# Kernel optimization log

Measured on AMD Instinct MI355X. Metric: run time of the kernel, lower is better.

## Reference

```python
import jax, jax.numpy as jnp
import numpy as np

B, S, D = 4, 2048, 1024
EPS = 1e-6


def setup_inputs() -> dict:
    key = jax.random.key(0)
    ks = jax.random.split(key, 9)
    s = 1.0 / np.sqrt(D)
    return {
        "context": jax.random.normal(ks[0], (B, S, D), jnp.float32),
        "eos_mask": jax.random.randint(ks[1], (B, S, S), 0, 2, dtype=jnp.int32),
        "prior": jax.random.uniform(ks[2], (B, S, S), jnp.float32),
        "Wq": jax.random.uniform(ks[3], (D, D), jnp.float32, -s, s),
        "bq": jax.random.uniform(ks[4], (D,), jnp.float32, -s, s),
        "Wk": jax.random.uniform(ks[5], (D, D), jnp.float32, -s, s),
        "bk": jax.random.uniform(ks[6], (D,), jnp.float32, -s, s),
        "gamma": jnp.ones((D,), jnp.float32),
        "beta": jnp.zeros((D,), jnp.float32),
    }


def reference(context, eos_mask, prior, Wq, bq, Wk, bk, gamma, beta):
    d = context.shape[-1]
    seq = context.shape[1]

    # LayerNorm with torch's unbiased std (Bessel correction)
    mean = jnp.mean(context, axis=-1, keepdims=True)
    var = jnp.sum((context - mean) ** 2, axis=-1, keepdims=True) / (d - 1)
    x = gamma * (context - mean) / (jnp.sqrt(var) + EPS) + beta

    q = x @ Wq + bq  # linear_query
    k = x @ Wk + bk  # linear_key

    scores = jnp.einsum("bid,bjd->bij", q, k) / d  # note: /d, not /sqrt(d)

    idx = jnp.arange(seq)
    band = jnp.abs(idx[:, None] - idx[None, :]) == 1      # a + c (tridiagonal off-diagonals)
    sup = (idx[None, :] - idx[:, None]) == 1              # a (superdiagonal)
    strict_upper = idx[:, None] < idx[None, :]            # triu(ones) - eye
    eye = idx[:, None] == idx[None, :]

    mask = (eos_mask != 0) & band[None]                   # eos_mask & (a + c)
    scores = jnp.where(mask, scores, -1e9)
    na = jax.nn.softmax(scores, axis=-1)
    na = jnp.sqrt(na * jnp.swapaxes(na, -1, -2) + 1e-9)
    na = prior + (1.0 - prior) * na                       # hier_add_index branch

    # t = log(na+eps).masked_fill(a==0,0) @ triu  ==  cumsum along last axis
    t = jnp.where(sup[None], jnp.log(na + 1e-9), 0.0)
    t = jnp.cumsum(t, axis=-1)
    # g = triu @ t  ==  reversed cumsum along axis -2
    g = jnp.cumsum(t[..., ::-1, :], axis=-2)[..., ::-1, :]
    g = jnp.where(strict_upper[None], jnp.exp(g), 0.0)

    g_attn = g + jnp.swapaxes(g, -1, -2) + jnp.where(eye[None], na, 1e-9)
    return (g_attn, na)
```

## Files before the change

### kernel.cpp

```cpp
#include <hip/hip_runtime.h>
#include <hip/hip_bf16.h>
#include <cmath>

#define BB 4
#define SS 2048
#define DD 1024
#define BS (BB*SS)
constexpr float EPS = 1e-6f;

typedef __attribute__((ext_vector_type(8))) short short8;
typedef __attribute__((ext_vector_type(4))) float floatx4;

__device__ inline float bf2f(unsigned short u) {
    unsigned v = ((unsigned)u) << 16;
    float f; __builtin_memcpy(&f, &v, 4);
    return f;
}

__global__ __launch_bounds__(256)
void prep_kernel(const float* __restrict__ Wq, const float* __restrict__ Wk,
                 const float* __restrict__ bq, const float* __restrict__ bk,
                 __hip_bfloat16* __restrict__ Wb, float* __restrict__ u,
                 float* __restrict__ v, float* __restrict__ cs,
                 float* __restrict__ sacc) {
    int blk = blockIdx.x;
    if (blk < 2048) {
        int idx = blk * 256 + threadIdx.x;
        const int half = DD * DD / 4;
        const float* src = (idx < half) ? Wk : Wq;
        int off = (idx < half) ? idx : idx - half;
        float4 val = ((const float4*)src)[off];
        union { ushort4 uu; __hip_bfloat16 h[4]; } pk;
        pk.h[0] = __float2bfloat16(val.x);
        pk.h[1] = __float2bfloat16(val.y);
        pk.h[2] = __float2bfloat16(val.z);
        pk.h[3] = __float2bfloat16(val.w);
        ((ushort4*)Wb)[idx] = pk.uu;
    } else if (blk < 2561) {
        int gid = (blk - 2048) * 4 + (threadIdx.x >> 6);
        int lane = threadIdx.x & 63;
        if (gid > 2048) return;
        const float* row; const float* vec; float* outp;
        if (gid < 1024)      { row = Wq + (size_t)gid * DD;          vec = bk; outp = u + gid; }
        else if (gid < 2048) { row = Wk + (size_t)(gid - 1024) * DD; vec = bq; outp = v + (gid - 1024); }
        else                 { row = bq;                             vec = bk; outp = cs; }
        float s = 0.f;
        #pragma unroll
        for (int k = 0; k < 4; ++k) {
            float4 a = ((const float4*)row)[lane * 4 + k];
            float4 b = ((const float4*)vec)[lane * 4 + k];
            s += a.x * b.x + a.y * b.y + a.z * b.z + a.w * b.w;
        }
        #pragma unroll
        for (int off = 32; off; off >>= 1) s += __shfl_down(s, off);
        if (lane == 0) *outp = s;
    } else {
        int idx = (blk - 2561) * 1024 + threadIdx.x * 4;
        *(float4*)(sacc + idx) = make_float4(0.f, 0.f, 0.f, 0.f);
    }
}

__global__ __launch_bounds__(256)
void ln_kernel(const float* __restrict__ ctx, const float* __restrict__ gamma,
               const float* __restrict__ beta, const float* __restrict__ u,
               const float* __restrict__ v, const float* __restrict__ cs,
               __hip_bfloat16* __restrict__ xo, float* __restrict__ alpha,
               float* __restrict__ betav) {
    int row = blockIdx.x;
    int t = threadIdx.x;
    const float* r = ctx + (size_t)row * DD;
    float4 val = ((const float4*)r)[t];
    float s1 = val.x + val.y + val.z + val.w;
    float s2 = val.x*val.x + val.y*val.y + val.z*val.z + val.w*val.w;
    #pragma unroll
    for (int off = 32; off; off >>= 1) {
        s1 += __shfl_down(s1, off);
        s2 += __shfl_down(s2, off);
    }
    __shared__ float ls1[4], ls2[4];
    int wid = t >> 6, lane = t & 63;
    if (lane == 0) { ls1[wid] = s1; ls2[wid] = s2; }
    __syncthreads();
    if (t == 0) {
        float a = ls1[0] + ls1[1] + ls1[2] + ls1[3];
        float b = ls2[0] + ls2[1] + ls2[2] + ls2[3];
        float mean = a / DD;
        float var = (b - a * a / DD) / (DD - 1);
        ls1[0] = mean;
        ls2[0] = 1.0f / (sqrtf(var) + EPS);
    }
    __syncthreads();
    float mean = ls1[0], rstd = ls2[0];
    float4 g = ((const float4*)gamma)[t];
    float4 be = ((const float4*)beta)[t];
    float nx0 = g.x * (val.x - mean) * rstd + be.x;
    float nx1 = g.y * (val.y - mean) * rstd + be.y;
    float nx2 = g.z * (val.z - mean) * rstd + be.z;
    float nx3 = g.w * (val.w - mean) * rstd + be.w;
    union { ushort4 uu; __hip_bfloat16 h[4]; } pk;
    pk.h[0] = __float2bfloat16(nx0);
    pk.h[1] = __float2bfloat16(nx1);
    pk.h[2] = __float2bfloat16(nx2);
    pk.h[3] = __float2bfloat16(nx3);
    ((ushort4*)(xo + (size_t)row * DD))[t] = pk.uu;
    float4 u4 = ((const float4*)u)[t];
    float4 v4 = ((const float4*)v)[t];
    float du = nx0 * u4.x + nx1 * u4.y + nx2 * u4.z + nx3 * u4.w;
    float dv = nx0 * v4.x + nx1 * v4.y + nx2 * v4.z + nx3 * v4.w;
    #pragma unroll
    for (int off = 32; off; off >>= 1) {
        du += __shfl_down(du, off);
        dv += __shfl_down(dv, off);
    }
    __syncthreads();
    if (lane == 0) { ls1[wid] = du; ls2[wid] = dv; }
    __syncthreads();
    if (t == 0) {
        alpha[row] = ls1[0] + ls1[1] + ls1[2] + ls1[3] + *cs;
        betav[row] = ls2[0] + ls2[1] + ls2[2] + ls2[3];
    }
}

__global__ __launch_bounds__(256)
void gemm64_mfma(const __hip_bfloat16* __restrict__ A,
                 const __hip_bfloat16* __restrict__ B,
                 __hip_bfloat16* __restrict__ C, int ldc) {
    __shared__ short As[64 * 64];
    __shared__ short Bs[64 * 64];
    int tid = threadIdx.x;
    int wave = tid >> 6;
    int lane = tid & 63;
    int q = lane >> 4, m16 = lane & 15;
    int srow = lane >> 3;
    int skoff = ((lane & 7) ^ srow) * 8;

    const __hip_bfloat16* gA = A + ((size_t)blockIdx.x * 64 + wave * 16 + srow) * DD + skoff;
    const __hip_bfloat16* gB = B + ((size_t)blockIdx.y * 64 + wave * 16 + srow) * DD + skoff;
    short* lA0 = As + (wave * 16) * 64;
    short* lA1 = As + (wave * 16 + 8) * 64;
    short* lB0 = Bs + (wave * 16) * 64;
    short* lB1 = Bs + (wave * 16 + 8) * 64;

    int swr = (m16 & 7) * 8;

    floatx4 acc[4] = {};
    for (int k0 = 0; k0 < DD; k0 += 64) {
        __builtin_amdgcn_global_load_lds(
            (const __attribute__((address_space(1))) void*)(gA + k0),
            (__attribute__((address_space(3))) void*)(lA0), 16, 0, 0);
        __builtin_amdgcn_global_load_lds(
            (const __attribute__((address_space(1))) void*)(gA + k0 + 8 * DD),
            (__attribute__((address_space(3))) void*)(lA1), 16, 0, 0);
        __builtin_amdgcn_global_load_lds(
            (const __attribute__((address_space(1))) void*)(gB + k0),
            (__attribute__((address_space(3))) void*)(lB0), 16, 0, 0);
        __builtin_amdgcn_global_load_lds(
            (const __attribute__((address_space(1))) void*)(gB + k0 + 8 * DD),
            (__attribute__((address_space(3))) void*)(lB1), 16, 0, 0);
        __syncthreads();
        #pragma unroll
        for (int h = 0; h < 2; ++h) {
            short8 af = *(const short8*)(As + (wave * 16 + m16) * 64 + ((h * 32 + q * 8) ^ swr));
            #pragma unroll
            for (int c = 0; c < 4; ++c) {
                short8 bf_ = *(const short8*)(Bs + (c * 16 + m16) * 64 + ((h * 32 + q * 8) ^ swr));
                acc[c] = __builtin_amdgcn_mfma_f32_16x16x32_bf16(af, bf_, acc[c], 0, 0, 0);
            }
        }
        __syncthreads();
    }
    #pragma unroll
    for (int c = 0; c < 4; ++c) {
        int gcol = blockIdx.y * 64 + c * 16 + m16;
        #pragma unroll
        for (int e = 0; e < 4; ++e) {
            int grow = blockIdx.x * 64 + wave * 16 + q * 4 + e;
            C[(size_t)grow * ldc + gcol] = __float2bfloat16(acc[c][e]);
        }
    }
}

#define TM 128
#define TN 128
#define BK 64
__global__ __launch_bounds__(256)
void gemm2_fused(const __hip_bfloat16* __restrict__ A,
                 const __hip_bfloat16* __restrict__ B,
                 float* __restrict__ sacc) {
    __shared__ short smem[32768];
    int tid = threadIdx.x;
    int wave = tid >> 6;
    int lane = tid & 63;
    int wm = wave >> 1, wn = wave & 1;
    int q = lane >> 4, m16 = lane & 15;

    int srow = lane >> 3;
    int skoff = ((lane & 7) ^ srow) * 8;
    const __hip_bfloat16* gA = A + ((size_t)blockIdx.x * TM + wave * 32 + srow) * DD + skoff;
    const __hip_bfloat16* gB = B + ((size_t)blockIdx.y * TN + wave * 32 + srow) * DD + skoff;

    int swr = (m16 & 7) * 8;

    floatx4 acc[4][4] = {};

    #define STAGE(p, k0) do {                                                        \
        short* As_ = smem + (p) * 16384;                                             \
        short* Bs_ = As_ + 8192;                                                     \
        _Pragma("unroll")                                                            \
        for (int i_ = 0; i_ < 4; ++i_) {                                             \
            __builtin_amdgcn_global_load_lds(                                        \
                (const __attribute__((address_space(1))) void*)(gA + (k0) + i_ * 8 * DD), \
                (__attribute__((address_space(3))) void*)(As_ + (wave * 32 + i_ * 8) * BK), 16, 0, 0); \
            __builtin_amdgcn_global_load_lds(                                        \
                (const __attribute__((address_space(1))) void*)(gB + (k0) + i_ * 8 * DD), \
                (__attribute__((address_space(3))) void*)(Bs_ + (wave * 32 + i_ * 8) * BK), 16, 0, 0); \
        }                                                                            \
    } while (0)

    #define COMPUTE(p) do {                                                          \
        const short* As_ = smem + (p) * 16384;                                       \
        const short* Bs_ = As_ + 8192;                                               \
        _Pragma("unroll")                                                            \
        for (int kk = 0; kk < 2; ++kk) {                                             \
            short8 af[4], bfr[4];                                                    \
            _Pragma("unroll")                                                        \
            for (int r = 0; r < 4; ++r)                                              \
                af[r] = *(const short8*)(As_ + (wm * 64 + r * 16 + m16) * BK + ((kk * 32 + q * 8) ^ swr)); \
            _Pragma("unroll")                                                        \
            for (int c = 0; c < 4; ++c)                                              \
                bfr[c] = *(const short8*)(Bs_ + (wn * 64 + c * 16 + m16) * BK + ((kk * 32 + q * 8) ^ swr)); \
            _Pragma("unroll")                                                        \
            for (int r = 0; r < 4; ++r)                                              \
                _Pragma("unroll")                                                    \
                for (int c = 0; c < 4; ++c)                                          \
                    acc[r][c] = __builtin_amdgcn_mfma_f32_16x16x32_bf16(af[r], bfr[c], acc[r][c], 0, 0, 0); \
        }                                                                            \
    } while (0)

    STAGE(0, 0);
    __syncthreads();
    for (int t = 0; t < DD / BK; t += 2) {
        if (t + 1 < DD / BK) STAGE(1, (t + 1) * BK);
        COMPUTE(0);
        __syncthreads();
        if (t + 2 < DD / BK) STAGE(0, (t + 2) * BK);
        COMPUTE(1);
        __syncthreads();
    }
    #undef STAGE
    #undef COMPUTE

    short* EP = smem + wave * 4608;
    #pragma unroll
    for (int r = 0; r < 4; ++r)
        #pragma unroll
        for (int c = 0; c < 4; ++c)
            #pragma unroll
            for (int e = 0; e < 4; ++e) {
                __hip_bfloat16 hv = __float2bfloat16(acc[r][c][e]);
                EP[(r * 16 + q * 4 + e) * 72 + c * 16 + m16] = *(short*)&hv;
            }

    int rl = lane;
    int growZ = blockIdx.x * TM + wm * 64 + rl;
    int gcol0 = blockIdx.y * TN + wn * 64;
    bool hs = (growZ + 1 < BS);
    bool hb = (growZ >= 1);
    const short8* psup = (const short8*)(A + (size_t)(growZ + 1) * DD + gcol0);
    const short8* psub = (const short8*)(A + (size_t)(growZ - 1) * DD + gcol0);
    float sup = 0.f, sub = 0.f;
    #pragma unroll
    for (int c8 = 0; c8 < 8; ++c8) {
        short8 zz = *(const short8*)(EP + rl * 72 + c8 * 8);
        float zf[8];
        #pragma unroll
        for (int e = 0; e < 8; ++e) zf[e] = bf2f((unsigned short)zz[e]);
        if (hs) {
            short8 xx = psup[c8];
            #pragma unroll
            for (int e = 0; e < 8; ++e) sup += zf[e] * bf2f((unsigned short)xx[e]);
        }
        if (hb) {
            short8 xx = psub[c8];
            #pragma unroll
            for (int e = 0; e < 8; ++e) sub += zf[e] * bf2f((unsigned short)xx[e]);
        }
    }
    if (hs) atomicAdd(&sacc[growZ], sup);
    if (hb) atomicAdd(&sacc[BS + growZ], sub);
}

__global__ __launch_bounds__(256)
void softmax_kernel(const float* __restrict__ sacc, const int* __restrict__ eos,
                    const float* __restrict__ alpha, const float* __restrict__ betav,
                    float* __restrict__ vsub, float* __restrict__ vsup,
                    float* __restrict__ wuni) {
    int gw = blockIdx.x * 256 + threadIdx.x;
    int i = gw & (SS - 1);
    float a = alpha[gw];
    float ssup = 0.f, ssub = 0.f;
    if (i < SS - 1) ssup = (sacc[gw] + a + betav[gw + 1]) * (1.0f / DD);
    if (i > 0)      ssub = (sacc[BS + gw] + a + betav[gw - 1]) * (1.0f / DD);
    bool msub = (i > 0) && (__builtin_nontemporal_load(&eos[(size_t)gw * SS + (i - 1)]) != 0);
    bool msup = (i < SS - 1) && (__builtin_nontemporal_load(&eos[(size_t)gw * SS + (i + 1)]) != 0);
    float vs, vp, w;
    if (msub && msup) {
        float mx = fmaxf(ssub, ssup);
        float e1 = expf(ssub - mx), e2 = expf(ssup - mx);
        float inv = 1.0f / (e1 + e2);
        vs = e1 * inv; vp = e2 * inv; w = 0.f;
    } else if (msub) { vs = 1.f; vp = 0.f; w = 0.f; }
    else if (msup)   { vs = 0.f; vp = 1.f; w = 0.f; }
    else             { vs = vp = w = 1.0f / SS; }
    vsub[gw] = vs; vsup[gw] = vp; wuni[gw] = w;
}

__global__ __launch_bounds__(256)
void scan_kernel(const float* __restrict__ prior, const float* __restrict__ vsub,
                 const float* __restrict__ vsup, double* __restrict__ Lc) {
    int b = blockIdx.x;
    int t = threadIdx.x;
    double loc[8];
    double s = 0.0;
    #pragma unroll
    for (int k = 0; k < 8; ++k) {
        int tt = t * 8 + k;
        double Lv = 0.0;
        if (tt < SS - 1) {
            float pr = prior[((size_t)(b * SS + tt)) * SS + tt + 1];
            float na2 = sqrtf(vsup[b * SS + tt] * vsub[b * SS + tt + 1] + 1e-9f);
            float P = pr + (1.f - pr) * na2;
            Lv = log((double)P + 1e-9);
        }
        loc[k] = Lv; s += Lv;
    }
    __shared__ double sa[256], sb[256];
    sa[t] = s;
    __syncthreads();
    double* src = sa; double* dst = sb;
    for (int off = 1; off < 256; off <<= 1) {
        double v = src[t];
        if (t >= off) v += src[t - off];
        __syncthreads();
        dst[t] = v;
        __syncthreads();
        double* tmp = src; src = dst; dst = tmp;
    }
    double run = (t == 0) ? 0.0 : src[t - 1];
    #pragma unroll
    for (int k = 0; k < 8; ++k) {
        int idx = t * 8 + k;
        Lc[b * SS + idx] = run;
        run += loc[k];
    }
}

__global__ __launch_bounds__(256)
void out_kernel(const float* __restrict__ prior, const float* __restrict__ vsub,
                const float* __restrict__ vsup, const float* __restrict__ wuni,
                const double* __restrict__ Lc, float* __restrict__ out_g,
                float* __restrict__ out_na) {
    size_t gid = (size_t)blockIdx.x * 256 + threadIdx.x;
    int jt = (int)(gid & 511);
    int row = (int)(gid >> 9);
    int i = row & (SS - 1);
    int b = row >> 11;
    int j0 = jt * 4;
    size_t base = (size_t)row * SS + j0;
    floatx4 pr4 = __builtin_nontemporal_load((const floatx4*)(prior + base));
    float4 wj4 = *(const float4*)(wuni + b * SS + j0);
    float pra[4] = {pr4.x, pr4.y, pr4.z, pr4.w};
    float wja[4] = {wj4.x, wj4.y, wj4.z, wj4.w};
    float wi = wuni[row];
    double Lci = Lc[row];
    const double* Lcb = Lc + b * SS;
    float nav[4], gv[4];
    #pragma unroll
    for (int c = 0; c < 4; ++c) {
        int j = j0 + c;
        float prod;
        if (j == i - 1)      prod = vsub[row] * vsup[row - 1];
        else if (j == i + 1) prod = vsup[row] * vsub[row + 1];
        else if (j == i)     prod = wi * wi;
        else                 prod = wi * wja[c];
        float na2 = sqrtf(prod + 1e-9f);
        float p = pra[c];
        float na3 = p + (1.f - p) * na2;
        nav[c] = na3;
        if (j == i) {
            gv[c] = na3;
        } else {
            double d = (j > i) ? (Lcb[j] - Lci) : (Lci - Lcb[j]);
            gv[c] = expf((float)d) + 1e-9f;
        }
    }
    floatx4 gq = { gv[0], gv[1], gv[2], gv[3] };
    floatx4 nq = { nav[0], nav[1], nav[2], nav[3] };
    __builtin_nontemporal_store(gq, (floatx4*)(out_g + base));
    __builtin_nontemporal_store(nq, (floatx4*)(out_na + base));
}

extern "C" void kernel_launch(void* const* d_in, const int* in_sizes, int n_in,
                              void* d_out, int out_size, void* d_ws, size_t ws_size,
                              hipStream_t stream) {
    const float* ctx   = (const float*)d_in[0];
    const int*   eos   = (const int*)d_in[1];
    const float* prior = (const float*)d_in[2];
    const float* Wq    = (const float*)d_in[3];
    const float* bq    = (const float*)d_in[4];
    const float* Wk    = (const float*)d_in[5];
    const float* bk    = (const float*)d_in[6];
    const float* gamma = (const float*)d_in[7];
    const float* beta  = (const float*)d_in[8];

    float* out_g  = (float*)d_out;
    float* out_na = out_g + (size_t)BB * SS * SS;

    char* ws = (char*)d_ws;
    size_t o = 0;
    __hip_bfloat16* x  = (__hip_bfloat16*)(ws + o); o += (size_t)BS * DD * 2;
    __hip_bfloat16* Wb = (__hip_bfloat16*)(ws + o); o += (size_t)2 * DD * DD * 2;
    __hip_bfloat16* Mt = (__hip_bfloat16*)(ws + o); o += (size_t)DD * DD * 2;
    double* Lc   = (double*)(ws + o); o += (size_t)BS * 8;
    float* u     = (float*)(ws + o);  o += DD * 4;
    float* v     = (float*)(ws + o);  o += DD * 4;
    float* cs    = (float*)(ws + o);  o += 64;
    float* alpha = (float*)(ws + o);  o += (size_t)BS * 4;
    float* betav = (float*)(ws + o);  o += (size_t)BS * 4;
    float* vsub  = (float*)(ws + o);  o += (size_t)BS * 4;
    float* vsup  = (float*)(ws + o);  o += (size_t)BS * 4;
    float* wuni  = (float*)(ws + o);  o += (size_t)BS * 4;
    float* sacc  = (float*)(ws + o);  o += (size_t)2 * BS * 4;

    __hip_bfloat16* Wk_bf = Wb;
    __hip_bfloat16* Wq_bf = Wb + (size_t)DD * DD;

    prep_kernel<<<2577, 256, 0, stream>>>(Wq, Wk, bq, bk, Wb, u, v, cs, sacc);
    ln_kernel<<<BS, 256, 0, stream>>>(ctx, gamma, beta, u, v, cs, x, alpha, betav);

    dim3 g1(DD / 64, DD / 64);
    gemm64_mfma<<<g1, 256, 0, stream>>>(Wk_bf, Wq_bf, Mt, DD);

    dim3 g2(BS / TM, DD / TN);
    gemm2_fused<<<g2, 256, 0, stream>>>(x, Mt, sacc);

    softmax_kernel<<<BS / 256, 256, 0, stream>>>(sacc, eos, alpha, betav, vsub, vsup, wuni);

    scan_kernel<<<BB, 256, 0, stream>>>(prior, vsub, vsup, Lc);

    size_t total = (size_t)BB * SS * SS / 4;
    out_kernel<<<(int)(total / 256), 256, 0, stream>>>(prior, vsub, vsup, wuni, Lc,
                                                       out_g, out_na);
}
```

Before: 322.8 us.

## Use wave-per-row LayerNorm, double-buffer small GEMM, shrink softmax blocks

```diff
diff --git a/kernel.cpp b/kernel.cpp
--- a/kernel.cpp
+++ b/kernel.cpp
@@ -66,58 +66,58 @@
                const float* __restrict__ v, const float* __restrict__ cs,
                __hip_bfloat16* __restrict__ xo, float* __restrict__ alpha,
                float* __restrict__ betav) {
-    int row = blockIdx.x;
-    int t = threadIdx.x;
-    const float* r = ctx + (size_t)row * DD;
-    float4 val = ((const float4*)r)[t];
-    float s1 = val.x + val.y + val.z + val.w;
-    float s2 = val.x*val.x + val.y*val.y + val.z*val.z + val.w*val.w;
+    int wid = threadIdx.x >> 6, lane = threadIdx.x & 63;
+    int row = blockIdx.x * 4 + wid;
+    const float4* r = (const float4*)(ctx + (size_t)row * DD);
+    float4 val[4];
+    float s1 = 0.f, s2 = 0.f;
+    #pragma unroll
+    for (int k = 0; k < 4; ++k) {
+        val[k] = r[lane + 64 * k];
+        s1 += val[k].x + val[k].y + val[k].z + val[k].w;
+        s2 += val[k].x * val[k].x + val[k].y * val[k].y
+            + val[k].z * val[k].z + val[k].w * val[k].w;
+    }
     #pragma unroll
     for (int off = 32; off; off >>= 1) {
         s1 += __shfl_down(s1, off);
         s2 += __shfl_down(s2, off);
     }
-    __shared__ float ls1[4], ls2[4];
-    int wid = t >> 6, lane = t & 63;
-    if (lane == 0) { ls1[wid] = s1; ls2[wid] = s2; }
-    __syncthreads();
-    if (t == 0) {
-        float a = ls1[0] + ls1[1] + ls1[2] + ls1[3];
-        float b = ls2[0] + ls2[1] + ls2[2] + ls2[3];
-        float mean = a / DD;
-        float var = (b - a * a / DD) / (DD - 1);
-        ls1[0] = mean;
-        ls2[0] = 1.0f / (sqrtf(var) + EPS);
-    }
-    __syncthreads();
-    float mean = ls1[0], rstd = ls2[0];
-    float4 g = ((const float4*)gamma)[t];
-    float4 be = ((const float4*)beta)[t];
-    float nx0 = g.x * (val.x - mean) * rstd + be.x;
-    float nx1 = g.y * (val.y - mean) * rstd + be.y;
-    float nx2 = g.z * (val.z - mean) * rstd + be.z;
-    float nx3 = g.w * (val.w - mean) * rstd + be.w;
-    union { ushort4 uu; __hip_bfloat16 h[4]; } pk;
-    pk.h[0] = __float2bfloat16(nx0);
-    pk.h[1] = __float2bfloat16(nx1);
-    pk.h[2] = __float2bfloat16(nx2);
-    pk.h[3] = __float2bfloat16(nx3);
-    ((ushort4*)(xo + (size_t)row * DD))[t] = pk.uu;
-    float4 u4 = ((const float4*)u)[t];
-    float4 v4 = ((const float4*)v)[t];
-    float du = nx0 * u4.x + nx1 * u4.y + nx2 * u4.z + nx3 * u4.w;
-    float dv = nx0 * v4.x + nx1 * v4.y + nx2 * v4.z + nx3 * v4.w;
+    s1 = __shfl(s1, 0);
+    s2 = __shfl(s2, 0);
+    float mean = s1 / DD;
+    float var  = (s2 - s1 * s1 / DD) / (DD - 1);
+    float rstd = 1.0f / (sqrtf(var) + EPS);
+    float du = 0.f, dv = 0.f;
+    ushort4* xout = (ushort4*)(xo + (size_t)row * DD);
+    #pragma unroll
+    for (int k = 0; k < 4; ++k) {
+        int idx = lane + 64 * k;
+        float4 g  = ((const float4*)gamma)[idx];
+        float4 be = ((const float4*)beta)[idx];
+        float nx0 = g.x * (val[k].x - mean) * rstd + be.x;
+        float nx1 = g.y * (val[k].y - mean) * rstd + be.y;
+        float nx2 = g.z * (val[k].z - mean) * rstd + be.z;
+        float nx3 = g.w * (val[k].w - mean) * rstd + be.w;
+        union { ushort4 uu; __hip_bfloat16 h[4]; } pk;
+        pk.h[0] = __float2bfloat16(nx0);
+        pk.h[1] = __float2bfloat16(nx1);
+        pk.h[2] = __float2bfloat16(nx2);
+        pk.h[3] = __float2bfloat16(nx3);
+        xout[idx] = pk.uu;
+        float4 u4 = ((const float4*)u)[idx];
+        float4 v4 = ((const float4*)v)[idx];
+        du += nx0 * u4.x + nx1 * u4.y + nx2 * u4.z + nx3 * u4.w;
+        dv += nx0 * v4.x + nx1 * v4.y + nx2 * v4.z + nx3 * v4.w;
+    }
     #pragma unroll
     for (int off = 32; off; off >>= 1) {
         du += __shfl_down(du, off);
         dv += __shfl_down(dv, off);
     }
-    __syncthreads();
-    if (lane == 0) { ls1[wid] = du; ls2[wid] = dv; }
-    __syncthreads();
-    if (t == 0) {
-        alpha[row] = ls1[0] + ls1[1] + ls1[2] + ls1[3] + *cs;
-        betav[row] = ls2[0] + ls2[1] + ls2[2] + ls2[3];
+    if (lane == 0) {
+        alpha[row] = du + *cs;
+        betav[row] = dv;
     }
 }
 
@@ -125,8 +125,7 @@
 void gemm64_mfma(const __hip_bfloat16* __restrict__ A,
                  const __hip_bfloat16* __restrict__ B,
                  __hip_bfloat16* __restrict__ C, int ldc) {
-    __shared__ short As[64 * 64];
-    __shared__ short Bs[64 * 64];
+    __shared__ short smem[16384];
     int tid = threadIdx.x;
     int wave = tid >> 6;
     int lane = tid & 63;
@@ -136,39 +135,55 @@
 
     const __hip_bfloat16* gA = A + ((size_t)blockIdx.x * 64 + wave * 16 + srow) * DD + skoff;
     const __hip_bfloat16* gB = B + ((size_t)blockIdx.y * 64 + wave * 16 + srow) * DD + skoff;
-    short* lA0 = As + (wave * 16) * 64;
-    short* lA1 = As + (wave * 16 + 8) * 64;
-    short* lB0 = Bs + (wave * 16) * 64;
-    short* lB1 = Bs + (wave * 16 + 8) * 64;
 
     int swr = (m16 & 7) * 8;
 
     floatx4 acc[4] = {};
-    for (int k0 = 0; k0 < DD; k0 += 64) {
-        __builtin_amdgcn_global_load_lds(
-            (const __attribute__((address_space(1))) void*)(gA + k0),
-            (__attribute__((address_space(3))) void*)(lA0), 16, 0, 0);
-        __builtin_amdgcn_global_load_lds(
-            (const __attribute__((address_space(1))) void*)(gA + k0 + 8 * DD),
-            (__attribute__((address_space(3))) void*)(lA1), 16, 0, 0);
-        __builtin_amdgcn_global_load_lds(
-            (const __attribute__((address_space(1))) void*)(gB + k0),
-            (__attribute__((address_space(3))) void*)(lB0), 16, 0, 0);
-        __builtin_amdgcn_global_load_lds(
-            (const __attribute__((address_space(1))) void*)(gB + k0 + 8 * DD),
-            (__attribute__((address_space(3))) void*)(lB1), 16, 0, 0);
-        __syncthreads();
-        #pragma unroll
-        for (int h = 0; h < 2; ++h) {
-            short8 af = *(const short8*)(As + (wave * 16 + m16) * 64 + ((h * 32 + q * 8) ^ swr));
-            #pragma unroll
-            for (int c = 0; c < 4; ++c) {
-                short8 bf_ = *(const short8*)(Bs + (c * 16 + m16) * 64 + ((h * 32 + q * 8) ^ swr));
-                acc[c] = __builtin_amdgcn_mfma_f32_16x16x32_bf16(af, bf_, acc[c], 0, 0, 0);
-            }
-        }
-        __syncthreads();
-    }
+
+    #define STG(p, k0) do {                                                          \
+        short* As_ = smem + (p) * 8192;                                              \
+        short* Bs_ = As_ + 4096;                                                     \
+        __builtin_amdgcn_global_load_lds(                                            \
+            (const __attribute__((address_space(1))) void*)(gA + (k0)),              \
+            (__attribute__((address_space(3))) void*)(As_ + (wave * 16) * 64), 16, 0, 0); \
+        __builtin_amdgcn_global_load_lds(                                            \
+            (const __attribute__((address_space(1))) void*)(gA + (k0) + 8 * DD),     \
+            (__attribute__((address_space(3))) void*)(As_ + (wave * 16 + 8) * 64), 16, 0, 0); \
+        __builtin_amdgcn_global_load_lds(                                            \
+            (const __attribute__((address_space(1))) void*)(gB + (k0)),              \
+            (__attribute__((address_space(3))) void*)(Bs_ + (wave * 16) * 64), 16, 0, 0); \
+        __builtin_amdgcn_global_load_lds(                                            \
+            (const __attribute__((address_space(1))) void*)(gB + (k0) + 8 * DD),     \
+            (__attribute__((address_space(3))) void*)(Bs_ + (wave * 16 + 8) * 64), 16, 0, 0); \
+    } while (0)
+
+    #define CMP(p) do {                                                              \
+        const short* As_ = smem + (p) * 8192;                                        \
+        const short* Bs_ = As_ + 4096;                                               \
+        _Pragma("unroll")                                                            \
+        for (int h = 0; h < 2; ++h) {                                                \
+            short8 af = *(const short8*)(As_ + (wave * 16 + m16) * 64 + ((h * 32 + q * 8) ^ swr)); \
+            _Pragma("unroll")                                                        \
+            for (int c = 0; c < 4; ++c) {                                            \
+                short8 bf_ = *(const short8*)(Bs_ + (c * 16 + m16) * 64 + ((h * 32 + q * 8) ^ swr)); \
+                acc[c] = __builtin_amdgcn_mfma_f32_16x16x32_bf16(af, bf_, acc[c], 0, 0, 0); \
+            }                                                                        \
+        }                                                                            \
+    } while (0)
+
+    STG(0, 0);
+    __syncthreads();
+    for (int k0 = 0; k0 < DD; k0 += 128) {
+        if (k0 + 64 < DD) STG(1, k0 + 64);
+        CMP(0);
+        __syncthreads();
+        if (k0 + 128 < DD) STG(0, k0 + 128);
+        CMP(1);
+        __syncthreads();
+    }
+    #undef STG
+    #undef CMP
+
     #pragma unroll
     for (int c = 0; c < 4; ++c) {
         int gcol = blockIdx.y * 64 + c * 16 + m16;
@@ -290,12 +305,12 @@
     if (hb) atomicAdd(&sacc[BS + growZ], sub);
 }
 
-__global__ __launch_bounds__(256)
+__global__ __launch_bounds__(64)
 void softmax_kernel(const float* __restrict__ sacc, const int* __restrict__ eos,
                     const float* __restrict__ alpha, const float* __restrict__ betav,
                     float* __restrict__ vsub, float* __restrict__ vsup,
                     float* __restrict__ wuni) {
-    int gw = blockIdx.x * 256 + threadIdx.x;
+    int gw = blockIdx.x * 64 + threadIdx.x;
     int i = gw & (SS - 1);
     float a = alpha[gw];
     float ssup = 0.f, ssub = 0.f;
@@ -436,7 +451,7 @@
     __hip_bfloat16* Wq_bf = Wb + (size_t)DD * DD;
 
     prep_kernel<<<2577, 256, 0, stream>>>(Wq, Wk, bq, bk, Wb, u, v, cs, sacc);
-    ln_kernel<<<BS, 256, 0, stream>>>(ctx, gamma, beta, u, v, cs, x, alpha, betav);
+    ln_kernel<<<BS / 4, 256, 0, stream>>>(ctx, gamma, beta, u, v, cs, x, alpha, betav);
 
     dim3 g1(DD / 64, DD / 64);
     gemm64_mfma<<<g1, 256, 0, stream>>>(Wk_bf, Wq_bf, Mt, DD);
@@ -444,7 +459,7 @@
     dim3 g2(BS / TM, DD / TN);
     gemm2_fused<<<g2, 256, 0, stream>>>(x, Mt, sacc);
 
-    softmax_kernel<<<BS / 256, 256, 0, stream>>>(sacc, eos, alpha, betav, vsub, vsup, wuni);
+    softmax_kernel<<<BS / 64, 64, 0, stream>>>(sacc, eos, alpha, betav, vsub, vsup, wuni);
 
     scan_kernel<<<BB, 256, 0, stream>>>(prior, vsub, vsup, Lc);
 
```

New measurement: 319.5 us. No clear change (-1.0%).
